# Performance work log

Measured on AMD Instinct MI355X. Metric: run time of the kernel, lower is better.

The kernel has to match this reference:

```python
import jax, jax.numpy as jnp
import numpy as np

EPS = 0.1
MAX_ITER = 10
N, IN_SIZE, IN_DIM = 16, 1024, 1024
HEADS, OUT_SIZE, OUT_DIM = 4, 128, 1024


def xavier(key, shape):
    fan_in, fan_out = shape[-1], int(np.prod(shape[:-1]))
    lim = float(np.sqrt(6.0 / (fan_in + fan_out)))
    return jax.random.uniform(key, shape, jnp.float32, -lim, lim)


def setup_inputs() -> dict:
    key = jax.random.key(0)
    k1, k2, k3 = jax.random.split(key, 3)
    x = jax.random.normal(k1, (N, IN_SIZE, IN_DIM), jnp.float32)
    ot_weight = xavier(k2, (HEADS, OUT_SIZE, IN_DIM))
    lin_w = xavier(k3, (OUT_DIM, HEADS * IN_DIM))
    lin_b = jnp.zeros((OUT_DIM,), jnp.float32)
    return {"x": x, "ot_weight": ot_weight, "lin_w": lin_w, "lin_b": lin_b}


def log_sinkhorn(K, max_iter):
    # K: [B, in_size, out_size] (already divided by eps)
    B, in_size, out_size = K.shape
    a = jnp.log(jnp.asarray(out_size / in_size, K.dtype))
    u = jnp.zeros((B, in_size), K.dtype)
    v = jnp.zeros((B, out_size), K.dtype)

    def body(carry, _):
        u, v = carry
        u = a - jax.nn.logsumexp(K + u[:, :, None] + v[:, None, :], axis=-1)
        v = -jax.nn.logsumexp(K + u[:, :, None] + v[:, None, :], axis=-2)
        return (u, v), None

    (u, v), _ = jax.lax.scan(body, (u, v), None, length=max_iter)
    return jnp.exp(K + u[:, :, None] + v[:, None, :])  # transport plan T


def reference(x, ot_weight, lin_w, lin_b):
    n, in_size, in_dim = x.shape
    m, out_size, _ = ot_weight.shape
    # similarity / eps : [n, m, in_size, out_size]
    K = jnp.einsum('nid,msd->nmis', x, ot_weight) / EPS
    T = log_sinkhorn(K.reshape(n * m, in_size, out_size), MAX_ITER)
    T = T.reshape(n, m, in_size, out_size)
    # weighted aggregation: [n, out_size, m, in_dim] -> [n, out_size, m*in_dim]
    feat = jnp.einsum('nmis,nid->nsmd', T, x).reshape(n, out_size, m * in_dim)
    # Linear + ReLU (Dropout is identity in eval mode)
    out = jax.nn.relu(feat @ lin_w.T + lin_b)
    return out
```

## Files before the change

### kernel.cpp

```cpp
#include <hip/hip_runtime.h>
#include <math.h>

#define EPSV 0.1f
#define MAX_ITER 10
constexpr int NB       = 16;
constexpr int IN_SIZE  = 1024;
constexpr int IN_DIM   = 1024;
constexpr int HEADS    = 4;
constexpr int OUT_SIZE = 128;
constexpr int OUT_DIM  = 1024;

typedef __attribute__((ext_vector_type(8))) _Float16 f16x8;
typedef __attribute__((ext_vector_type(4))) float f32x4;

__device__ __forceinline__ unsigned cvth2(float lo, float hi) {
    _Float16 a = (_Float16)lo, b = (_Float16)hi;
    unsigned short ua = *(unsigned short*)&a, ub = *(unsigned short*)&b;
    return (unsigned)ua | ((unsigned)ub << 16);
}
__device__ __forceinline__ unsigned short cvth1(float f) {
    _Float16 a = (_Float16)f;
    return *(unsigned short*)&a;
}
__device__ __forceinline__ unsigned short bf16rne(float f) {
    unsigned a = __float_as_uint(f);
    return (unsigned short)((a + 0x7fffu + ((a >> 16) & 1u)) >> 16);
}
__device__ __forceinline__ void glds16(const void* g, void* l) {
    __builtin_amdgcn_global_load_lds(
        (const __attribute__((address_space(1))) unsigned int*)g,
        (__attribute__((address_space(3))) unsigned int*)l, 16, 0, 0);
}

template<bool B_F32, int CMODE, int NF, bool SWAP, bool HMAP>
__global__ __launch_bounds__(256)
void mfma_gemm(const void* __restrict__ Ap, const void* __restrict__ Bp,
               const float* __restrict__ bias, void* __restrict__ Cp,
               int K, int lda, int ldb, int ldc, int div,
               long AsN, long AsM, long BsN, long BsM, long CsN, long CsM,
               float alpha)
{
    constexpr int BN   = NF * 32;
    constexpr int BSTR = B_F32 ? 40 : 32;
    const int z  = SWAP ? blockIdx.x : blockIdx.z;
    const int n0 = (SWAP ? blockIdx.z : blockIdx.x) * BN;
    long aoff, boff, coff;
    if (HMAP) {
        const int nn = z & 15, mm = z >> 4, bt = nn * 4 + mm;
        aoff = (long)bt * AsM; boff = (long)nn * BsN; coff = (long)bt * CsM;
    } else {
        aoff = (long)(z / div) * AsN + (long)(z % div) * AsM;
        boff = (long)(z / div) * BsN + (long)(z % div) * BsM;
        coff = (long)(z / div) * CsN + (long)(z % div) * CsM;
    }

    __shared__ short As[2][128 * 32];
    __shared__ short Bs[2][BN * BSTR];

    const int t = threadIdx.x;
    const int lane = t & 63;
    const int w = t >> 6, wr = w >> 1, wc = w & 1;
    const int lrow = lane >> 2, lce = (lane & 3) * 8;

    auto stage = [&](int buf, int k0) {
        const long abase = aoff + k0;
        const long bbase = boff + k0;
        #pragma unroll
        for (int j = 0; j < 2; ++j) {
            const int row0 = (w * 2 + j) * 16;
            glds16((const short*)Ap + abase + (long)(row0 + lrow) * lda + lce,
                   &As[buf][row0 * 32]);
        }
        if (B_F32) {
            #pragma unroll
            for (int itr = 0; itr < BN / 64; ++itr) {
                const int idx = itr * 256 + t;
                const int row = idx >> 2, kq = idx & 3;
                const float* s = (const float*)Bp + bbase + (long)(n0 + row) * ldb + kq * 8;
                const float4 f0 = *(const float4*)s, f1 = *(const float4*)(s + 4);
                uint4 p;
                p.x = cvth2(f0.x, f0.y); p.y = cvth2(f0.z, f0.w);
                p.z = cvth2(f1.x, f1.y); p.w = cvth2(f1.z, f1.w);
                *(uint4*)&Bs[buf][row * BSTR + kq * 8] = p;
            }
        } else {
            #pragma unroll
            for (int j = 0; j < BN / 64; ++j) {
                const int row0 = (w * (BN / 64) + j) * 16;
                glds16((const short*)Bp + bbase + (long)(n0 + row0 + lrow) * ldb + lce,
                       &Bs[buf][row0 * 32]);
            }
        }
    };

    f32x4 acc[4][NF];
    #pragma unroll
    for (int i = 0; i < 4; ++i)
        #pragma unroll
        for (int j = 0; j < NF; ++j) { acc[i][j].x = 0.f; acc[i][j].y = 0.f; acc[i][j].z = 0.f; acc[i][j].w = 0.f; }

    stage(0, 0);
    __syncthreads();
    int cur = 0;

    for (int k0 = 0; k0 < K; k0 += 32) {
        if (k0 + 32 < K) stage(cur ^ 1, k0 + 32);

        f16x8 af[4], bfr[NF];
        #pragma unroll
        for (int mi = 0; mi < 4; ++mi)
            af[mi] = *(const f16x8*)&As[cur][(wr * 64 + mi * 16 + (lane & 15)) * 32 + (lane >> 4) * 8];
        #pragma unroll
        for (int ni = 0; ni < NF; ++ni)
            bfr[ni] = *(const f16x8*)&Bs[cur][(wc * (BN / 2) + ni * 16 + (lane & 15)) * BSTR + (lane >> 4) * 8];
        #pragma unroll
        for (int mi = 0; mi < 4; ++mi)
            #pragma unroll
            for (int ni = 0; ni < NF; ++ni)
                acc[mi][ni] = __builtin_amdgcn_mfma_f32_16x16x32_f16(af[mi], bfr[ni], acc[mi][ni], 0, 0, 0);
        __syncthreads();
        cur ^= 1;
    }

    #pragma unroll
    for (int mi = 0; mi < 4; ++mi) {
        #pragma unroll
        for (int ni = 0; ni < NF; ++ni) {
            #pragma unroll
            for (int j = 0; j < 4; ++j) {
                const int row = wr * 64 + mi * 16 + (lane >> 4) * 4 + j;
                const int col = n0 + wc * (BN / 2) + ni * 16 + (lane & 15);
                float v = acc[mi][ni][j] * alpha;
                if (CMODE == 2) { v += bias[col]; v = fmaxf(v, 0.f); }
                if (CMODE == 2) ((float*)Cp)[coff + (long)row * ldc + col] = v;
                else ((unsigned short*)Cp)[coff + (long)row * ldc + col] = cvth1(v);
            }
        }
    }
}

__global__ __launch_bounds__(256)
void splitk_reduce(const unsigned short* __restrict__ part,
                   const float* __restrict__ bias, float* __restrict__ out)
{
    const long idx = ((long)blockIdx.x * 256 + threadIdx.x) * 8;
    const int o = (int)(idx & 1023);
    const f16x8 p0 = *(const f16x8*)(part + idx);
    const f16x8 p1 = *(const f16x8*)(part + 2097152 + idx);
    const f16x8 p2 = *(const f16x8*)(part + 2 * 2097152 + idx);
    const f16x8 p3 = *(const f16x8*)(part + 3 * 2097152 + idx);
    const float4 b0 = *(const float4*)(bias + o);
    const float4 b1 = *(const float4*)(bias + o + 4);
    float r[8];
    #pragma unroll
    for (int j = 0; j < 8; ++j) {
        const float bv = j < 4 ? (&b0.x)[j] : (&b1.x)[j - 4];
        r[j] = fmaxf((float)p0[j] + (float)p1[j] + (float)p2[j] + (float)p3[j] + bv, 0.f);
    }
    *(float4*)(out + idx)     = *(float4*)&r[0];
    *(float4*)(out + idx + 4) = *(float4*)&r[4];
}

__global__ __launch_bounds__(256)
void cvt_f16(const float* __restrict__ in, unsigned short* __restrict__ out)
{
    const long i8 = ((long)blockIdx.x * 256 + threadIdx.x) * 8;
    const float4 f0 = *(const float4*)(in + i8), f1 = *(const float4*)(in + i8 + 4);
    uint4 p;
    p.x = cvth2(f0.x, f0.y); p.y = cvth2(f0.z, f0.w);
    p.z = cvth2(f1.x, f1.y); p.w = cvth2(f1.z, f1.w);
    *(uint4*)(out + i8) = p;
}

__global__ __launch_bounds__(256)
void gemm1_exp(const unsigned short* __restrict__ otwH, const float* __restrict__ x,
               unsigned short* __restrict__ ekb, float* __restrict__ MiB)
{
    const int zb = blockIdx.x;
    const int nn = zb & 15, mm = zb >> 4;
    const int bt = nn * 4 + mm;
    const unsigned short* A = otwH + (long)mm * (OUT_SIZE * IN_DIM);
    const float* B = x + (long)nn * (IN_SIZE * IN_DIM);
    const int n0 = blockIdx.z * 128;

    __shared__ short As[2][128 * 32];
    __shared__ short Bs[2][128 * 40];
    __shared__ float colmax[2][128];

    const int t = threadIdx.x;
    const int lane = t & 63;
    const int w = t >> 6, wr = w >> 1, wc = w & 1;
    const int lrow = lane >> 2, lce = (lane & 3) * 8;

    auto stage = [&](int buf, int k0) {
        #pragma unroll
        for (int j = 0; j < 2; ++j) {
            const int row0 = (w * 2 + j) * 16;
            glds16(A + (long)(row0 + lrow) * 1024 + k0 + lce, &As[buf][row0 * 32]);
        }
        #pragma unroll
        for (int itr = 0; itr < 2; ++itr) {
            const int idx = itr * 256 + t;
            const int row = idx >> 2, kq = idx & 3;
            const float* s = B + (long)(n0 + row) * 1024 + k0 + kq * 8;
            const float4 f0 = *(const float4*)s, f1 = *(const float4*)(s + 4);
            uint4 p;
            p.x = cvth2(f0.x, f0.y); p.y = cvth2(f0.z, f0.w);
            p.z = cvth2(f1.x, f1.y); p.w = cvth2(f1.z, f1.w);
            *(uint4*)&Bs[buf][row * 40 + kq * 8] = p;
        }
    };

    f32x4 acc[4][4];
    #pragma unroll
    for (int i = 0; i < 4; ++i)
        #pragma unroll
        for (int j = 0; j < 4; ++j) { acc[i][j].x = 0.f; acc[i][j].y = 0.f; acc[i][j].z = 0.f; acc[i][j].w = 0.f; }

    stage(0, 0);
    __syncthreads();
    int cur = 0;

    for (int k0 = 0; k0 < 1024; k0 += 32) {
        if (k0 + 32 < 1024) stage(cur ^ 1, k0 + 32);

        f16x8 af[4], bfr[4];
        #pragma unroll
        for (int mi = 0; mi < 4; ++mi)
            af[mi] = *(const f16x8*)&As[cur][(wr * 64 + mi * 16 + (lane & 15)) * 32 + (lane >> 4) * 8];
        #pragma unroll
        for (int ni = 0; ni < 4; ++ni)
            bfr[ni] = *(const f16x8*)&Bs[cur][(wc * 64 + ni * 16 + (lane & 15)) * 40 + (lane >> 4) * 8];
        #pragma unroll
        for (int mi = 0; mi < 4; ++mi)
            #pragma unroll
            for (int ni = 0; ni < 4; ++ni)
                acc[mi][ni] = __builtin_amdgcn_mfma_f32_16x16x32_f16(af[mi], bfr[ni], acc[mi][ni], 0, 0, 0);
        __syncthreads();
        cur ^= 1;
    }

    float lm[4];
    #pragma unroll
    for (int ni = 0; ni < 4; ++ni) {
        float mx = -INFINITY;
        #pragma unroll
        for (int mi = 0; mi < 4; ++mi)
            #pragma unroll
            for (int j = 0; j < 4; ++j) mx = fmaxf(mx, acc[mi][ni][j]);
        mx *= 10.0f;
        mx = fmaxf(mx, __shfl_xor(mx, 16, 64));
        mx = fmaxf(mx, __shfl_xor(mx, 32, 64));
        lm[ni] = mx;
    }
    if ((lane >> 4) == 0) {
        #pragma unroll
        for (int ni = 0; ni < 4; ++ni) colmax[wr][wc * 64 + ni * 16 + lane] = lm[ni];
    }
    __syncthreads();
    float cm[4];
    #pragma unroll
    for (int ni = 0; ni < 4; ++ni) {
        const int c = wc * 64 + ni * 16 + (lane & 15);
        cm[ni] = fmaxf(colmax[0][c], colmax[1][c]);
    }
    if (wr == 0 && (lane >> 4) == 0) {
        #pragma unroll
        for (int ni = 0; ni < 4; ++ni)
            MiB[(long)bt * 1024 + n0 + wc * 64 + ni * 16 + lane] = cm[ni];
    }
    unsigned short* ekz = ekb + (long)bt * (OUT_SIZE * IN_SIZE);
    #pragma unroll
    for (int mi = 0; mi < 4; ++mi) {
        #pragma unroll
        for (int ni = 0; ni < 4; ++ni) {
            const int col = n0 + wc * 64 + ni * 16 + (lane & 15);
            #pragma unroll
            for (int j = 0; j < 4; ++j) {
                const int row = wr * 64 + mi * 16 + (lane >> 4) * 4 + j;
                ekz[(long)row * 1024 + col] = bf16rne(__expf(fmaf(acc[mi][ni][j], 10.f, -cm[ni])));
            }
        }
    }
}

__global__ __launch_bounds__(256)
void transpose_cvt(const float* __restrict__ x, unsigned short* __restrict__ xT)
{
    const int n = blockIdx.z, i0 = blockIdx.y * 64, d0 = blockIdx.x * 64;
    const float* xs = x + (long)n * (IN_SIZE * IN_DIM);
    unsigned short* xo = xT + (long)n * (IN_SIZE * IN_DIM);
    __shared__ float tile[64][65];
    const int t = threadIdx.x;
    const int r = t >> 4, c4 = (t & 15) * 4;
    #pragma unroll
    for (int rr = 0; rr < 4; ++rr) {
        const float4 v = *(const float4*)(xs + (long)(i0 + rr * 16 + r) * IN_DIM + d0 + c4);
        *(float4*)&tile[rr * 16 + r][c4] = v;
    }
    __syncthreads();
    #pragma unroll
    for (int rr = 0; rr < 4; ++rr) {
        const int dl = rr * 16 + r;
        ushort4 o;
        o.x = cvth1(tile[c4 + 0][dl]); o.y = cvth1(tile[c4 + 1][dl]);
        o.z = cvth1(tile[c4 + 2][dl]); o.w = cvth1(tile[c4 + 3][dl]);
        *(ushort4*)(xo + (long)(d0 + dl) * IN_SIZE + i0 + c4) = o;
    }
}

__global__ __launch_bounds__(1024)
void sinkhorn_split(unsigned short* __restrict__ ekb,
                    const float* __restrict__ MiB,
                    float* __restrict__ xchg, unsigned int* __restrict__ ctr)
{
    const int b = blockIdx.x;
    const int q = blockIdx.z;
    const int t = threadIdx.x;
    const int lane = t & 63, w = t >> 6;

    __shared__ unsigned ekw[128 * 129];
    __shared__ float part_u[8][256];
    __shared__ float part_v[8][128];
    __shared__ float eu_l[256];
    __shared__ float v_s[128], ev_s[128];
    __shared__ float red8[8];
    __shared__ float wg_s;

    {
        const unsigned short* src = ekb + (long)b * 131072 + q * 256;
        #pragma unroll
        for (int j = 0; j < 4; ++j) {
            const int idx = t + 1024 * j;
            const int s = idx >> 5, c8 = (idx & 31) * 8;
            const uint4 p = *(const uint4*)(src + (long)s * 1024 + c8);
            const int bd = s * 129 + (c8 >> 1);
            ekw[bd] = p.x; ekw[bd + 1] = p.y; ekw[bd + 2] = p.z; ekw[bd + 3] = p.w;
        }
    }
    float mi_t = 0.f, u_reg = 0.f, w_t = 0.f;
    if (t < 256) mi_t = MiB[(long)b * 1024 + q * 256 + t];
    if (t < 128) { v_s[t] = 0.f; ev_s[t] = 1.0f; }
    __syncthreads();

    const float A0 = -2.0794415416798357f;
    float vmx = 0.f;

    for (int it = 0; it < MAX_ITER; ++it) {
        {
            const int p = t & 127, sq = t >> 7;
            float s0 = 0.f, s1 = 0.f;
            #pragma unroll
            for (int j = 0; j < 16; ++j) {
                const int s = sq * 16 + j;
                const unsigned e = ekw[s * 129 + p];
                const float evv = ev_s[s];
                s0 = fmaf(__uint_as_float(e << 16),          evv, s0);
                s1 = fmaf(__uint_as_float(e & 0xffff0000u),  evv, s1);
            }
            part_u[sq][2 * p]     = s0;
            part_u[sq][2 * p + 1] = s1;
        }
        __syncthreads();

        if (t < 256) {
            float S = part_u[0][t];
            #pragma unroll
            for (int g = 1; g < 8; ++g) S += part_u[g][t];
            const float un = A0 - u_reg - mi_t - vmx - __logf(S);
            u_reg = un;
            w_t = mi_t + un;
            float wl = w_t;
            #pragma unroll
            for (int m = 1; m < 64; m <<= 1) wl = fmaxf(wl, __shfl_xor(wl, m, 64));
            if (lane == 0) red8[4 + w] = wl;
        }
        __syncthreads();
        const float wmx_l = fmaxf(fmaxf(red8[4], red8[5]), fmaxf(red8[6], red8[7]));
        if (t < 256) eu_l[t] = __expf(w_t - wmx_l);
        __syncthreads();

        {
            const int s = t & 127, g = t >> 7;
            float acc = 0.f;
            #pragma unroll
            for (int j = 0; j < 16; ++j) {
                const int p = 16 * g + j;
                const unsigned e = ekw[s * 129 + p];
                const float2 eup = *(const float2*)&eu_l[2 * p];
                acc = fmaf(__uint_as_float(e << 16),         eup.x, acc);
                acc = fmaf(__uint_as_float(e & 0xffff0000u), eup.y, acc);
            }
            part_v[g][s] = acc;
        }
        __syncthreads();

        float* slot = xchg + ((long)(b * MAX_ITER + it) * 4 + q) * 160;
        if (t < 128) {
            float cp_l = part_v[0][t];
            #pragma unroll
            for (int g = 1; g < 8; ++g) cp_l += part_v[g][t];
            __hip_atomic_store(slot + t, cp_l, __ATOMIC_RELAXED, __HIP_MEMORY_SCOPE_AGENT);
        }
        if (t == 0)
            __hip_atomic_store(slot + 128, wmx_l, __ATOMIC_RELAXED, __HIP_MEMORY_SCOPE_AGENT);
        __syncthreads();
        if (t == 0) {
            unsigned int* c = ctr + b * MAX_ITER + it;
            __hip_atomic_fetch_add(c, 1u, __ATOMIC_RELEASE, __HIP_MEMORY_SCOPE_AGENT);
            while (__hip_atomic_load(c, __ATOMIC_RELAXED, __HIP_MEMORY_SCOPE_AGENT) < 4u) {}
            (void)__hip_atomic_load(c, __ATOMIC_ACQUIRE, __HIP_MEMORY_SCOPE_AGENT);
        }
        __syncthreads();

        if (t < 128) {
            float* base = xchg + (long)(b * MAX_ITER + it) * 4 * 160;
            const float w0 = __hip_atomic_load(base + 0 * 160 + 128, __ATOMIC_RELAXED, __HIP_MEMORY_SCOPE_AGENT);
            const float w1 = __hip_atomic_load(base + 1 * 160 + 128, __ATOMIC_RELAXED, __HIP_MEMORY_SCOPE_AGENT);
            const float w2 = __hip_atomic_load(base + 2 * 160 + 128, __ATOMIC_RELAXED, __HIP_MEMORY_SCOPE_AGENT);
            const float w3 = __hip_atomic_load(base + 3 * 160 + 128, __ATOMIC_RELAXED, __HIP_MEMORY_SCOPE_AGENT);
            const float wg = fmaxf(fmaxf(w0, w1), fmaxf(w2, w3));
            const float c0 = __hip_atomic_load(base + 0 * 160 + t, __ATOMIC_RELAXED, __HIP_MEMORY_SCOPE_AGENT);
            const float c1 = __hip_atomic_load(base + 1 * 160 + t, __ATOMIC_RELAXED, __HIP_MEMORY_SCOPE_AGENT);
            const float c2 = __hip_atomic_load(base + 2 * 160 + t, __ATOMIC_RELAXED, __HIP_MEMORY_SCOPE_AGENT);
            const float c3 = __hip_atomic_load(base + 3 * 160 + t, __ATOMIC_RELAXED, __HIP_MEMORY_SCOPE_AGENT);
            const float cp = c0 * __expf(w0 - wg) + c1 * __expf(w1 - wg)
                           + c2 * __expf(w2 - wg) + c3 * __expf(w3 - wg);
            const float vn = -v_s[t] - wg - __logf(cp);
            v_s[t] = vn;
            if (t == 0) wg_s = wg;
            float xv = vn;
            #pragma unroll
            for (int m = 1; m < 64; m <<= 1) xv = fmaxf(xv, __shfl_xor(xv, m, 64));
            if (lane == 0) red8[w] = xv;
        }
        __syncthreads();
        vmx = fmaxf(red8[0], red8[1]);
        if (t < 128) ev_s[t] = __expf(v_s[t] - vmx);
        __syncthreads();
    }

    const float wg = wg_s;
    if (t < 256) eu_l[t] = __expf(w_t - wg);
    if (t < 128) ev_s[t] = __expf(v_s[t] + wg);
    __syncthreads();
    unsigned short* To = ekb + (long)b * 131072 + q * 256;
    #pragma unroll
    for (int j = 0; j < 16; ++j) {
        const int idx = t + 1024 * j;
        const int s  = idx >> 7;
        const int ip = idx & 127;
        const unsigned e = ekw[s * 129 + ip];
        const float2 eup = *(const float2*)&eu_l[2 * ip];
        const float ec = ev_s[s];
        const float lo = __uint_as_float(e << 16)         * eup.x * ec;
        const float hi = __uint_as_float(e & 0xffff0000u) * eup.y * ec;
        *(unsigned*)(To + (long)s * 1024 + ip * 2) = cvth2(lo, hi);
    }
}

extern "C" void kernel_launch(void* const* d_in, const int* in_sizes, int n_in,
                              void* d_out, int out_size, void* d_ws, size_t ws_size,
                              hipStream_t stream)
{
    const float* x     = (const float*)d_in[0];
    const float* otw   = (const float*)d_in[1];
    const float* lin_w = (const float*)d_in[2];
    const float* lin_b = (const float*)d_in[3];
    float* out = (float*)d_out;

    unsigned short* xT   = (unsigned short*)d_ws;
    unsigned short* ekb  = xT + 16777216;
    unsigned short* feat = ekb + 8388608;
    unsigned short* partial = (unsigned short*)d_ws;
    float* MiB  = (float*)d_out;
    float* xchg = MiB + 131072;
    unsigned int* ctrB = (unsigned int*)(MiB + 655360);
    unsigned short* otwH = (unsigned short*)(MiB + 786432);

    hipMemsetAsync(ctrB, 0, 64 * MAX_ITER * sizeof(unsigned int), stream);

    cvt_f16<<<dim3(256), 256, 0, stream>>>(otw, otwH);

    gemm1_exp<<<dim3(64, 1, 8), 256, 0, stream>>>(otwH, x, ekb, MiB);

    transpose_cvt<<<dim3(16, 16, NB), 256, 0, stream>>>(x, xT);

    sinkhorn_split<<<dim3(64, 1, 4), 1024, 0, stream>>>(ekb, MiB, xchg, ctrB);

    mfma_gemm<false, 1, 2, true, true><<<dim3(64, 1, 16), 256, 0, stream>>>(
        ekb, xT, nullptr, feat,
        1024, 1024, 1024, 1024, 4,
        0, 131072, 1048576, 0, 0, 131072, 1.0f);

    mfma_gemm<true, 1, 2, false, false><<<dim3(16, 1, 64), 256, 0, stream>>>(
        feat, lin_w, nullptr, partial,
        1024, 1024, 4096, 1024, 16,
        131072, 524288, 1024, 0, 2097152, 131072, 1.0f);

    splitk_reduce<<<dim3(1024), 256, 0, stream>>>(partial, lin_b, out);
}
```

Measured before the change: 188.7 us.

## Split gemm1 and Sinkhorn across twice as many blocks with smaller tiles

The first GEMM+exp kernel now uses 64-column tiles, so it launches 1024 blocks instead of 512. The cooperative Sinkhorn kernel now splits each batch across 8 blocks of 512 threads instead of 4 blocks of 1024 threads, each holding 128 columns in shared memory. The cross-block exchange and spin barrier now wait for 8 participants, and the workspace offsets are moved to fit the larger exchange buffer. This raises parallelism and CU occupancy on the latency-bound iterative phase. In exchange, the GEMM gets less data reuse per block and every Sinkhorn iteration carries more global synchronisation traffic, and the spin barrier requires all 512 blocks to be resident at once.

```diff
diff --git a/kernel.cpp b/kernel.cpp
--- a/kernel.cpp
+++ b/kernel.cpp
@@ -181,11 +181,11 @@
     const int bt = nn * 4 + mm;
     const unsigned short* A = otwH + (long)mm * (OUT_SIZE * IN_DIM);
     const float* B = x + (long)nn * (IN_SIZE * IN_DIM);
-    const int n0 = blockIdx.z * 128;
+    const int n0 = blockIdx.z * 64;
 
     __shared__ short As[2][128 * 32];
-    __shared__ short Bs[2][128 * 40];
-    __shared__ float colmax[2][128];
+    __shared__ short Bs[2][64 * 40];
+    __shared__ float colmax[2][64];
 
     const int t = threadIdx.x;
     const int lane = t & 63;
@@ -198,10 +198,8 @@
             const int row0 = (w * 2 + j) * 16;
             glds16(A + (long)(row0 + lrow) * 1024 + k0 + lce, &As[buf][row0 * 32]);
         }
-        #pragma unroll
-        for (int itr = 0; itr < 2; ++itr) {
-            const int idx = itr * 256 + t;
-            const int row = idx >> 2, kq = idx & 3;
+        {
+            const int row = t >> 2, kq = t & 3;
             const float* s = B + (long)(n0 + row) * 1024 + k0 + kq * 8;
             const float4 f0 = *(const float4*)s, f1 = *(const float4*)(s + 4);
             uint4 p;
@@ -211,11 +209,11 @@
         }
     };
 
-    f32x4 acc[4][4];
+    f32x4 acc[4][2];
     #pragma unroll
     for (int i = 0; i < 4; ++i)
         #pragma unroll
-        for (int j = 0; j < 4; ++j) { acc[i][j].x = 0.f; acc[i][j].y = 0.f; acc[i][j].z = 0.f; acc[i][j].w = 0.f; }
+        for (int j = 0; j < 2; ++j) { acc[i][j].x = 0.f; acc[i][j].y = 0.f; acc[i][j].z = 0.f; acc[i][j].w = 0.f; }
 
     stage(0, 0);
     __syncthreads();
@@ -224,25 +222,25 @@
     for (int k0 = 0; k0 < 1024; k0 += 32) {
         if (k0 + 32 < 1024) stage(cur ^ 1, k0 + 32);
 
-        f16x8 af[4], bfr[4];
+        f16x8 af[4], bfr[2];
         #pragma unroll
         for (int mi = 0; mi < 4; ++mi)
             af[mi] = *(const f16x8*)&As[cur][(wr * 64 + mi * 16 + (lane & 15)) * 32 + (lane >> 4) * 8];
         #pragma unroll
-        for (int ni = 0; ni < 4; ++ni)
-            bfr[ni] = *(const f16x8*)&Bs[cur][(wc * 64 + ni * 16 + (lane & 15)) * 40 + (lane >> 4) * 8];
+        for (int ni = 0; ni < 2; ++ni)
+            bfr[ni] = *(const f16x8*)&Bs[cur][(wc * 32 + ni * 16 + (lane & 15)) * 40 + (lane >> 4) * 8];
         #pragma unroll
         for (int mi = 0; mi < 4; ++mi)
             #pragma unroll
-            for (int ni = 0; ni < 4; ++ni)
+            for (int ni = 0; ni < 2; ++ni)
                 acc[mi][ni] = __builtin_amdgcn_mfma_f32_16x16x32_f16(af[mi], bfr[ni], acc[mi][ni], 0, 0, 0);
         __syncthreads();
         cur ^= 1;
     }
 
-    float lm[4];
-    #pragma unroll
-    for (int ni = 0; ni < 4; ++ni) {
+    float lm[2];
+    #pragma unroll
+    for (int ni = 0; ni < 2; ++ni) {
         float mx = -INFINITY;
         #pragma unroll
         for (int mi = 0; mi < 4; ++mi)
@@ -255,26 +253,26 @@
     }
     if ((lane >> 4) == 0) {
         #pragma unroll
-        for (int ni = 0; ni < 4; ++ni) colmax[wr][wc * 64 + ni * 16 + lane] = lm[ni];
+        for (int ni = 0; ni < 2; ++ni) colmax[wr][wc * 32 + ni * 16 + lane] = lm[ni];
     }
     __syncthreads();
-    float cm[4];
-    #pragma unroll
-    for (int ni = 0; ni < 4; ++ni) {
-        const int c = wc * 64 + ni * 16 + (lane & 15);
+    float cm[2];
+    #pragma unroll
+    for (int ni = 0; ni < 2; ++ni) {
+        const int c = wc * 32 + ni * 16 + (lane & 15);
         cm[ni] = fmaxf(colmax[0][c], colmax[1][c]);
     }
     if (wr == 0 && (lane >> 4) == 0) {
         #pragma unroll
-        for (int ni = 0; ni < 4; ++ni)
-            MiB[(long)bt * 1024 + n0 + wc * 64 + ni * 16 + lane] = cm[ni];
+        for (int ni = 0; ni < 2; ++ni)
+            MiB[(long)bt * 1024 + n0 + wc * 32 + ni * 16 + lane] = cm[ni];
     }
     unsigned short* ekz = ekb + (long)bt * (OUT_SIZE * IN_SIZE);
     #pragma unroll
     for (int mi = 0; mi < 4; ++mi) {
         #pragma unroll
-        for (int ni = 0; ni < 4; ++ni) {
-            const int col = n0 + wc * 64 + ni * 16 + (lane & 15);
+        for (int ni = 0; ni < 2; ++ni) {
+            const int col = n0 + wc * 32 + ni * 16 + (lane & 15);
             #pragma unroll
             for (int j = 0; j < 4; ++j) {
                 const int row = wr * 64 + mi * 16 + (lane >> 4) * 4 + j;
@@ -309,7 +307,7 @@
     }
 }
 
-__global__ __launch_bounds__(1024)
+__global__ __launch_bounds__(512)
 void sinkhorn_split(unsigned short* __restrict__ ekb,
                     const float* __restrict__ MiB,
                     float* __restrict__ xchg, unsigned int* __restrict__ ctr)
@@ -319,27 +317,27 @@
     const int t = threadIdx.x;
     const int lane = t & 63, w = t >> 6;
 
-    __shared__ unsigned ekw[128 * 129];
-    __shared__ float part_u[8][256];
-    __shared__ float part_v[8][128];
-    __shared__ float eu_l[256];
+    __shared__ unsigned ekw[128 * 65];
+    __shared__ float part_u[8][128];
+    __shared__ float part_v[4][128];
+    __shared__ float eu_l[128];
     __shared__ float v_s[128], ev_s[128];
     __shared__ float red8[8];
     __shared__ float wg_s;
 
     {
-        const unsigned short* src = ekb + (long)b * 131072 + q * 256;
+        const unsigned short* src = ekb + (long)b * 131072 + q * 128;
         #pragma unroll
         for (int j = 0; j < 4; ++j) {
-            const int idx = t + 1024 * j;
-            const int s = idx >> 5, c8 = (idx & 31) * 8;
-            const uint4 p = *(const uint4*)(src + (long)s * 1024 + c8);
-            const int bd = s * 129 + (c8 >> 1);
+            const int idx = t + 512 * j;
+            const int s = idx >> 4, c16 = (idx & 15) * 8;
+            const uint4 p = *(const uint4*)(src + (long)s * 1024 + c16);
+            const int bd = s * 65 + (c16 >> 1);
             ekw[bd] = p.x; ekw[bd + 1] = p.y; ekw[bd + 2] = p.z; ekw[bd + 3] = p.w;
         }
     }
     float mi_t = 0.f, u_reg = 0.f, w_t = 0.f;
-    if (t < 256) mi_t = MiB[(long)b * 1024 + q * 256 + t];
+    if (t < 128) mi_t = MiB[(long)b * 1024 + q * 128 + t];
     if (t < 128) { v_s[t] = 0.f; ev_s[t] = 1.0f; }
     __syncthreads();
 
@@ -348,12 +346,12 @@
 
     for (int it = 0; it < MAX_ITER; ++it) {
         {
-            const int p = t & 127, sq = t >> 7;
+            const int p = t & 63, sq = t >> 6;
             float s0 = 0.f, s1 = 0.f;
             #pragma unroll
             for (int j = 0; j < 16; ++j) {
                 const int s = sq * 16 + j;
-                const unsigned e = ekw[s * 129 + p];
+                const unsigned e = ekw[s * 65 + p];
                 const float evv = ev_s[s];
                 s0 = fmaf(__uint_as_float(e << 16),          evv, s0);
                 s1 = fmaf(__uint_as_float(e & 0xffff0000u),  evv, s1);
@@ -363,7 +361,7 @@
         }
         __syncthreads();
 
-        if (t < 256) {
+        if (t < 128) {
             float S = part_u[0][t];
             #pragma unroll
             for (int g = 1; g < 8; ++g) S += part_u[g][t];
@@ -376,8 +374,8 @@
             if (lane == 0) red8[4 + w] = wl;
         }
         __syncthreads();
-        const float wmx_l = fmaxf(fmaxf(red8[4], red8[5]), fmaxf(red8[6], red8[7]));
-        if (t < 256) eu_l[t] = __expf(w_t - wmx_l);
+        const float wmx_l = fmaxf(red8[4], red8[5]);
+        if (t < 128) eu_l[t] = __expf(w_t - wmx_l);
         __syncthreads();
 
         {
@@ -386,7 +384,7 @@
             #pragma unroll
             for (int j = 0; j < 16; ++j) {
                 const int p = 16 * g + j;
-                const unsigned e = ekw[s * 129 + p];
+                const unsigned e = ekw[s * 65 + p];
                 const float2 eup = *(const float2*)&eu_l[2 * p];
                 acc = fmaf(__uint_as_float(e << 16),         eup.x, acc);
                 acc = fmaf(__uint_as_float(e & 0xffff0000u), eup.y, acc);
@@ -395,11 +393,9 @@
         }
         __syncthreads();
 
-        float* slot = xchg + ((long)(b * MAX_ITER + it) * 4 + q) * 160;
+        float* slot = xchg + ((long)(b * MAX_ITER + it) * 8 + q) * 160;
         if (t < 128) {
-            float cp_l = part_v[0][t];
-            #pragma unroll
-            for (int g = 1; g < 8; ++g) cp_l += part_v[g][t];
+            const float cp_l = part_v[0][t] + part_v[1][t] + part_v[2][t] + part_v[3][t];
             __hip_atomic_store(slot + t, cp_l, __ATOMIC_RELAXED, __HIP_MEMORY_SCOPE_AGENT);
         }
         if (t == 0)
@@ -408,24 +404,26 @@
         if (t == 0) {
             unsigned int* c = ctr + b * MAX_ITER + it;
             __hip_atomic_fetch_add(c, 1u, __ATOMIC_RELEASE, __HIP_MEMORY_SCOPE_AGENT);
-            while (__hip_atomic_load(c, __ATOMIC_RELAXED, __HIP_MEMORY_SCOPE_AGENT) < 4u) {}
+            while (__hip_atomic_load(c, __ATOMIC_RELAXED, __HIP_MEMORY_SCOPE_AGENT) < 8u) {}
             (void)__hip_atomic_load(c, __ATOMIC_ACQUIRE, __HIP_MEMORY_SCOPE_AGENT);
         }
         __syncthreads();
 
         if (t < 128) {
-            float* base = xchg + (long)(b * MAX_ITER + it) * 4 * 160;
-            const float w0 = __hip_atomic_load(base + 0 * 160 + 128, __ATOMIC_RELAXED, __HIP_MEMORY_SCOPE_AGENT);
-            const float w1 = __hip_atomic_load(base + 1 * 160 + 128, __ATOMIC_RELAXED, __HIP_MEMORY_SCOPE_AGENT);
-            const float w2 = __hip_atomic_load(base + 2 * 160 + 128, __ATOMIC_RELAXED, __HIP_MEMORY_SCOPE_AGENT);
-            const float w3 = __hip_atomic_load(base + 3 * 160 + 128, __ATOMIC_RELAXED, __HIP_MEMORY_SCOPE_AGENT);
-            const float wg = fmaxf(fmaxf(w0, w1), fmaxf(w2, w3));
-            const float c0 = __hip_atomic_load(base + 0 * 160 + t, __ATOMIC_RELAXED, __HIP_MEMORY_SCOPE_AGENT);
-            const float c1 = __hip_atomic_load(base + 1 * 160 + t, __ATOMIC_RELAXED, __HIP_MEMORY_SCOPE_AGENT);
-            const float c2 = __hip_atomic_load(base + 2 * 160 + t, __ATOMIC_RELAXED, __HIP_MEMORY_SCOPE_AGENT);
-            const float c3 = __hip_atomic_load(base + 3 * 160 + t, __ATOMIC_RELAXED, __HIP_MEMORY_SCOPE_AGENT);
-            const float cp = c0 * __expf(w0 - wg) + c1 * __expf(w1 - wg)
-                           + c2 * __expf(w2 - wg) + c3 * __expf(w3 - wg);
+            float* base = xchg + (long)(b * MAX_ITER + it) * 8 * 160;
+            float wq[8];
+            #pragma unroll
+            for (int g = 0; g < 8; ++g)
+                wq[g] = __hip_atomic_load(base + g * 160 + 128, __ATOMIC_RELAXED, __HIP_MEMORY_SCOPE_AGENT);
+            float wg = wq[0];
+            #pragma unroll
+            for (int g = 1; g < 8; ++g) wg = fmaxf(wg, wq[g]);
+            float cp = 0.f;
+            #pragma unroll
+            for (int g = 0; g < 8; ++g) {
+                const float cg = __hip_atomic_load(base + g * 160 + t, __ATOMIC_RELAXED, __HIP_MEMORY_SCOPE_AGENT);
+                cp = fmaf(cg, __expf(wq[g] - wg), cp);
+            }
             const float vn = -v_s[t] - wg - __logf(cp);
             v_s[t] = vn;
             if (t == 0) wg_s = wg;
@@ -441,16 +439,16 @@
     }
 
     const float wg = wg_s;
-    if (t < 256) eu_l[t] = __expf(w_t - wg);
+    if (t < 128) eu_l[t] = __expf(w_t - wg);
     if (t < 128) ev_s[t] = __expf(v_s[t] + wg);
     __syncthreads();
-    unsigned short* To = ekb + (long)b * 131072 + q * 256;
+    unsigned short* To = ekb + (long)b * 131072 + q * 128;
     #pragma unroll
     for (int j = 0; j < 16; ++j) {
-        const int idx = t + 1024 * j;
-        const int s  = idx >> 7;
-        const int ip = idx & 127;
-        const unsigned e = ekw[s * 129 + ip];
+        const int idx = t + 512 * j;
+        const int s  = idx >> 6;
+        const int ip = idx & 63;
+        const unsigned e = ekw[s * 65 + ip];
         const float2 eup = *(const float2*)&eu_l[2 * ip];
         const float ec = ev_s[s];
         const float lo = __uint_as_float(e << 16)         * eup.x * ec;
@@ -475,18 +473,18 @@
     unsigned short* partial = (unsigned short*)d_ws;
     float* MiB  = (float*)d_out;
     float* xchg = MiB + 131072;
-    unsigned int* ctrB = (unsigned int*)(MiB + 655360);
-    unsigned short* otwH = (unsigned short*)(MiB + 786432);
+    unsigned int* ctrB = (unsigned int*)(MiB + 950272);
+    unsigned short* otwH = (unsigned short*)(MiB + 951040);
 
     hipMemsetAsync(ctrB, 0, 64 * MAX_ITER * sizeof(unsigned int), stream);
 
     cvt_f16<<<dim3(256), 256, 0, stream>>>(otw, otwH);
 
-    gemm1_exp<<<dim3(64, 1, 8), 256, 0, stream>>>(otwH, x, ekb, MiB);
+    gemm1_exp<<<dim3(64, 1, 16), 256, 0, stream>>>(otwH, x, ekb, MiB);
 
     transpose_cvt<<<dim3(16, 16, NB), 256, 0, stream>>>(x, xT);
 
-    sinkhorn_split<<<dim3(64, 1, 4), 1024, 0, stream>>>(ekb, MiB, xchg, ctrB);
+    sinkhorn_split<<<dim3(64, 1, 8), 512, 0, stream>>>(ekb, MiB, xchg, ctrB);
 
     mfma_gemm<false, 1, 2, true, true><<<dim3(64, 1, 16), 256, 0, stream>>>(
         ekb, xT, nullptr, feat,
```

Result: slower. 230.6 us (+22.2%).

## Fuse x transpose-to-fp16 into gemm1 staging, drop transpose kernel

Applied to the files above, without the earlier changes.

The separate transpose_cvt kernel, which re-read the whole fp32 x tensor, is removed. gemm1_exp already stages x tiles as fp16 in shared memory, so it now writes the transposed fp16 copy (xT) straight from those tiles. Each head block handles one quarter of the K range, so the work is split across the four head blocks that share the same batch. This saves a full pass over x and one kernel launch. In exchange, gemm1's main loop gets extra strided shared-memory reads and global stores in a quarter of its iterations, and register pressure rises.

```diff
diff --git a/kernel.cpp b/kernel.cpp
--- a/kernel.cpp
+++ b/kernel.cpp
@@ -174,7 +174,8 @@
 
 __global__ __launch_bounds__(256)
 void gemm1_exp(const unsigned short* __restrict__ otwH, const float* __restrict__ x,
-               unsigned short* __restrict__ ekb, float* __restrict__ MiB)
+               unsigned short* __restrict__ ekb, float* __restrict__ MiB,
+               unsigned short* __restrict__ xTo)
 {
     const int zb = blockIdx.x;
     const int nn = zb & 15, mm = zb >> 4;
@@ -221,6 +222,8 @@
     __syncthreads();
     int cur = 0;
 
+    unsigned short* xTn = xTo + (long)nn * (IN_SIZE * IN_DIM);
+
     for (int k0 = 0; k0 < 1024; k0 += 32) {
         if (k0 + 32 < 1024) stage(cur ^ 1, k0 + 32);
 
@@ -236,6 +239,18 @@
             #pragma unroll
             for (int ni = 0; ni < 4; ++ni)
                 acc[mi][ni] = __builtin_amdgcn_mfma_f32_16x16x32_f16(af[mi], bfr[ni], acc[mi][ni], 0, 0, 0);
+
+        if ((k0 >> 8) == mm) {
+            const int dl = t & 31;
+            const int ig = (t >> 5) * 16;
+            unsigned short tmp[16];
+            #pragma unroll
+            for (int j = 0; j < 16; ++j)
+                tmp[j] = (unsigned short)Bs[cur][(ig + j) * 40 + dl];
+            unsigned short* dst = xTn + (long)(k0 + dl) * IN_SIZE + n0 + ig;
+            *(uint4*)dst       = *(uint4*)&tmp[0];
+            *(uint4*)(dst + 8) = *(uint4*)&tmp[8];
+        }
         __syncthreads();
         cur ^= 1;
     }
@@ -281,31 +296,6 @@
                 ekz[(long)row * 1024 + col] = bf16rne(__expf(fmaf(acc[mi][ni][j], 10.f, -cm[ni])));
             }
         }
-    }
-}
-
-__global__ __launch_bounds__(256)
-void transpose_cvt(const float* __restrict__ x, unsigned short* __restrict__ xT)
-{
-    const int n = blockIdx.z, i0 = blockIdx.y * 64, d0 = blockIdx.x * 64;
-    const float* xs = x + (long)n * (IN_SIZE * IN_DIM);
-    unsigned short* xo = xT + (long)n * (IN_SIZE * IN_DIM);
-    __shared__ float tile[64][65];
-    const int t = threadIdx.x;
-    const int r = t >> 4, c4 = (t & 15) * 4;
-    #pragma unroll
-    for (int rr = 0; rr < 4; ++rr) {
-        const float4 v = *(const float4*)(xs + (long)(i0 + rr * 16 + r) * IN_DIM + d0 + c4);
-        *(float4*)&tile[rr * 16 + r][c4] = v;
-    }
-    __syncthreads();
-    #pragma unroll
-    for (int rr = 0; rr < 4; ++rr) {
-        const int dl = rr * 16 + r;
-        ushort4 o;
-        o.x = cvth1(tile[c4 + 0][dl]); o.y = cvth1(tile[c4 + 1][dl]);
-        o.z = cvth1(tile[c4 + 2][dl]); o.w = cvth1(tile[c4 + 3][dl]);
-        *(ushort4*)(xo + (long)(d0 + dl) * IN_SIZE + i0 + c4) = o;
     }
 }
 
@@ -482,9 +472,7 @@
 
     cvt_f16<<<dim3(256), 256, 0, stream>>>(otw, otwH);
 
-    gemm1_exp<<<dim3(64, 1, 8), 256, 0, stream>>>(otwH, x, ekb, MiB);
-
-    transpose_cvt<<<dim3(16, 16, NB), 256, 0, stream>>>(x, xT);
+    gemm1_exp<<<dim3(64, 1, 8), 256, 0, stream>>>(otwH, x, ekb, MiB, xT);
 
     sinkhorn_split<<<dim3(64, 1, 4), 1024, 0, stream>>>(ekb, MiB, xchg, ctrB);
 
```

Result: faster. 175.3 us, median of 2 (-7.1%).
